# Kernel tuning notes

Measured on AMD Instinct MI355X. Metric: run time of the kernel, lower is better.

The kernel has to match this reference:

```python
import jax, jax.numpy as jnp
import numpy as np

HIDDEN = 2048
NUM_HEADS = 16
HEAD_DIM = HIDDEN // NUM_HEADS  # 128
SCALE = HEAD_DIM ** -0.5


def setup_inputs() -> dict:
    key = jax.random.key(0)
    ks = jax.random.split(key, 5)
    B, S = 2, 2048
    init = HIDDEN ** -0.5  # roughly kaiming-uniform scale for Linear weights
    return {
        "hidden_states": jax.random.normal(ks[0], (B, S, HIDDEN), dtype=jnp.float32),
        "Wq": jax.random.normal(ks[1], (HIDDEN, HIDDEN), dtype=jnp.float32) * init,
        "Wk": jax.random.normal(ks[2], (HIDDEN, HIDDEN), dtype=jnp.float32) * init,
        "Wv": jax.random.normal(ks[3], (HIDDEN, HIDDEN), dtype=jnp.float32) * init,
        "Wo": jax.random.normal(ks[4], (HIDDEN, HIDDEN), dtype=jnp.float32) * init,
    }


def reference(hidden_states, Wq, Wk, Wv, Wo):
    B, S, _ = hidden_states.shape
    # Projections (nn.Linear: x @ W.T; weights stored as [out, in])
    q = (hidden_states @ Wq.T).reshape(B, S, NUM_HEADS, HEAD_DIM).transpose(0, 2, 1, 3)
    k = (hidden_states @ Wk.T).reshape(B, S, NUM_HEADS, HEAD_DIM).transpose(0, 2, 1, 3)
    v = (hidden_states @ Wv.T).reshape(B, S, NUM_HEADS, HEAD_DIM).transpose(0, 2, 1, 3)
    # Full quadratic attention (faithful to the source's explicit materialization)
    scores = jnp.einsum("bhqd,bhkd->bhqk", q, k) * SCALE  # [B,H,S,S]
    probs = jax.nn.softmax(scores, axis=-1)
    attn = jnp.einsum("bhqk,bhkd->bhqd", probs, v)  # [B,H,S,Dh]
    attn = attn.transpose(0, 2, 1, 3).reshape(B, S, HIDDEN)
    return attn @ Wo.T
```

## Files before the change

### kernel.cpp

```cpp
#include <hip/hip_runtime.h>
#include <cstdint>

#define HIDDEN 2048
#define NHEADS 16
#define DH 128
#define BATCH 2
#define SEQ 2048
#define MTOT 4096
#define BH (BATCH * NHEADS)

typedef __attribute__((ext_vector_type(8))) short bf16x8;
typedef __attribute__((ext_vector_type(4))) float f32x4;

static constexpr float QSCALE = (float)(0.08838834764831845 * 1.4426950408889634);

__device__ __forceinline__ unsigned short f2bf(float f) {
  union { float f; uint32_t u; } v; v.f = f;
  uint32_t r = v.u + 0x7FFFu + ((v.u >> 16) & 1u);
  return (unsigned short)(r >> 16);
}
__device__ __forceinline__ uint32_t cvtpk(float lo, float hi) {
  uint32_t r;
  asm("v_cvt_pk_bf16_f32 %0, %1, %2" : "=v"(r) : "v"(lo), "v"(hi));
  return r;
}
__device__ __forceinline__ f32x4 mfma16(bf16x8 a, bf16x8 b, f32x4 c) {
  return __builtin_amdgcn_mfma_f32_16x16x32_bf16(a, b, c, 0, 0, 0);
}

typedef const __attribute__((address_space(1))) unsigned char* gas1_t;
typedef __attribute__((address_space(3))) unsigned char* las3_t;
__device__ __forceinline__ void gll16(const void* g, void* l) {
  __builtin_amdgcn_global_load_lds((gas1_t)g, (las3_t)l, 16, 0, 0);
}

template <int N>
__device__ __forceinline__ void waitvm() {
  if constexpr (N == 6) asm volatile("s_waitcnt vmcnt(6)" ::: "memory");
  else if constexpr (N == 3) asm volatile("s_waitcnt vmcnt(3)" ::: "memory");
  else asm volatile("s_waitcnt vmcnt(0)" ::: "memory");
}

__global__ __launch_bounds__(256) void cast_bf16_kernel(const float* __restrict__ in,
                                                        unsigned short* __restrict__ out,
                                                        int n) {
  int i = (blockIdx.x * 256 + threadIdx.x) * 4;
  if (i < n) {
    float4 f = *(const float4*)&in[i];
    ushort4 o;
    o.x = f2bf(f.x); o.y = f2bf(f.y); o.z = f2bf(f.z); o.w = f2bf(f.w);
    *(ushort4*)&out[i] = o;
  }
}

template <int VM>
__device__ __forceinline__ void gemm_body(int kt, char* SM,
                                          const unsigned short* pA,
                                          const unsigned short* pB0,
                                          const unsigned short* pB1,
                                          int wv, int wr, int wc, int g, int lr,
                                          f32x4 (&acc)[4][4]) {
  waitvm<VM>();
  __builtin_amdgcn_s_barrier();
  if (kt + 3 < 64) {
    char* slot = SM + ((kt + 3) & 3) * 24576;
    const size_t ko = (size_t)(kt + 3) * 32;
    gll16(pA + ko, slot + wv * 1024);
    gll16(pB0 + ko, slot + 8192 + wv * 1024);
    gll16(pB1 + ko, slot + 16384 + wv * 1024);
  }
  const char* Ac = SM + (kt & 3) * 24576;
  const char* Bc = Ac + 8192;
  const int fx = (lr >> 1) & 3;
  bf16x8 af[4], bfr[4];
#pragma unroll
  for (int mi = 0; mi < 4; ++mi)
    af[mi] = *(const bf16x8*)(Ac + (wr * 64 + mi * 16 + lr) * 64 + ((g ^ fx) * 16));
#pragma unroll
  for (int ni = 0; ni < 4; ++ni)
    bfr[ni] = *(const bf16x8*)(Bc + (wc * 64 + ni * 16 + lr) * 64 + ((g ^ fx) * 16));
  __builtin_amdgcn_s_setprio(1);
#pragma unroll
  for (int mi = 0; mi < 4; ++mi)
#pragma unroll
    for (int ni = 0; ni < 4; ++ni)
      acc[mi][ni] = mfma16(af[mi], bfr[ni], acc[mi][ni]);
  __builtin_amdgcn_s_setprio(0);
}

__global__ __launch_bounds__(512) void gemm_qkv_pipe(const unsigned short* __restrict__ A,
                                                     const unsigned short* __restrict__ Wq,
                                                     const unsigned short* __restrict__ Wk,
                                                     const unsigned short* __restrict__ Wv,
                                                     unsigned short* __restrict__ Qb,
                                                     unsigned short* __restrict__ Kb,
                                                     unsigned short* __restrict__ Vb) {
  __shared__ __align__(16) char SM[98304];
  const int tid = threadIdx.x;
  const int lane = tid & 63, wv = tid >> 6;
  const int wr = wv >> 2, wc = wv & 3;
  const int g = lane >> 4, lr = lane & 15;
  const int which = blockIdx.x >> 3;
  const int m0 = blockIdx.y * 128, n0 = (blockIdx.x & 7) * 256;
  const unsigned short* W = (which == 0) ? Wq : (which == 1) ? Wk : Wv;

  const int rA = tid >> 2, cA = (tid & 3) ^ ((rA >> 1) & 3);
  const unsigned short* pA = A + (size_t)(m0 + rA) * HIDDEN + cA * 8;
  const unsigned short* pB0 = W + (size_t)(n0 + rA) * HIDDEN + cA * 8;
  const unsigned short* pB1 = W + (size_t)(n0 + 128 + rA) * HIDDEN + cA * 8;

  f32x4 acc[4][4];
#pragma unroll
  for (int i = 0; i < 4; ++i)
#pragma unroll
    for (int j = 0; j < 4; ++j) acc[i][j] = (f32x4){0.f, 0.f, 0.f, 0.f};

#pragma unroll
  for (int t = 0; t < 3; ++t) {
    char* slot = SM + t * 24576;
    gll16(pA + t * 32, slot + wv * 1024);
    gll16(pB0 + t * 32, slot + 8192 + wv * 1024);
    gll16(pB1 + t * 32, slot + 16384 + wv * 1024);
  }

  for (int kt = 0; kt < 62; ++kt)
    gemm_body<6>(kt, SM, pA, pB0, pB1, wv, wr, wc, g, lr, acc);
  gemm_body<3>(62, SM, pA, pB0, pB1, wv, wr, wc, g, lr, acc);
  gemm_body<0>(63, SM, pA, pB0, pB1, wv, wr, wc, g, lr, acc);

  const float alpha = (which == 0) ? QSCALE : 1.0f;
  unsigned short* C = (which == 0) ? Qb : (which == 1) ? Kb : Vb;
#pragma unroll
  for (int mi = 0; mi < 4; ++mi)
#pragma unroll
    for (int ni = 0; ni < 4; ++ni)
#pragma unroll
      for (int r = 0; r < 4; ++r) {
        const int row = m0 + wr * 64 + mi * 16 + g * 4 + r;
        const int col = n0 + wc * 64 + ni * 16 + lr;
        const unsigned short v = f2bf(acc[mi][ni][r] * alpha);
        const int b = row >> 11, s = row & (SEQ - 1);
        const int h = col >> 7, d = col & (DH - 1);
        const size_t base = (size_t)(b * NHEADS + h) * SEQ * DH;
        if (which == 0)
          C[base + (size_t)s * DH + d] = v;
        else if (which == 1)
          C[base + (size_t)(s >> 5) * 4096 + (d >> 3) * 256 + (s & 31) * 8 + (d & 7)] = v;
        else
          C[base + (size_t)(s >> 3) * 1024 + d * 8 + (s & 7)] = v;
      }
}

__global__ __launch_bounds__(512) void gemm_out_pipe(const unsigned short* __restrict__ A,
                                                     const unsigned short* __restrict__ W,
                                                     float* __restrict__ C) {
  __shared__ __align__(16) char SM[98304];
  const int tid = threadIdx.x;
  const int lane = tid & 63, wv = tid >> 6;
  const int wr = wv >> 2, wc = wv & 3;
  const int g = lane >> 4, lr = lane & 15;
  const int m0 = blockIdx.y * 128, n0 = blockIdx.x * 256;

  const int rA = tid >> 2, cA = (tid & 3) ^ ((rA >> 1) & 3);
  const unsigned short* pA = A + (size_t)(m0 + rA) * HIDDEN + cA * 8;
  const unsigned short* pB0 = W + (size_t)(n0 + rA) * HIDDEN + cA * 8;
  const unsigned short* pB1 = W + (size_t)(n0 + 128 + rA) * HIDDEN + cA * 8;

  f32x4 acc[4][4];
#pragma unroll
  for (int i = 0; i < 4; ++i)
#pragma unroll
    for (int j = 0; j < 4; ++j) acc[i][j] = (f32x4){0.f, 0.f, 0.f, 0.f};

#pragma unroll
  for (int t = 0; t < 3; ++t) {
    char* slot = SM + t * 24576;
    gll16(pA + t * 32, slot + wv * 1024);
    gll16(pB0 + t * 32, slot + 8192 + wv * 1024);
    gll16(pB1 + t * 32, slot + 16384 + wv * 1024);
  }

  for (int kt = 0; kt < 62; ++kt)
    gemm_body<6>(kt, SM, pA, pB0, pB1, wv, wr, wc, g, lr, acc);
  gemm_body<3>(62, SM, pA, pB0, pB1, wv, wr, wc, g, lr, acc);
  gemm_body<0>(63, SM, pA, pB0, pB1, wv, wr, wc, g, lr, acc);

#pragma unroll
  for (int mi = 0; mi < 4; ++mi)
#pragma unroll
    for (int ni = 0; ni < 4; ++ni)
#pragma unroll
      for (int r = 0; r < 4; ++r) {
        const int row = m0 + wr * 64 + mi * 16 + g * 4 + r;
        const int col = n0 + wc * 64 + ni * 16 + lr;
        C[(size_t)row * HIDDEN + col] = acc[mi][ni][r];
      }
}

__global__ __launch_bounds__(256, 3) void attn_mfma(const unsigned short* __restrict__ Q,
                                                    const unsigned short* __restrict__ K,
                                                    const unsigned short* __restrict__ V,
                                                    unsigned short* __restrict__ Ab) {
  const int bid = blockIdx.x;
  const int bh = bid & 31;
  const int q0 = (bid >> 5) * 128;
  const int tid = threadIdx.x;
  const int wv = tid >> 6, lane = tid & 63;
  const int g = lane >> 4, lr = lane & 15;
  const unsigned short* Qh = Q + (size_t)bh * SEQ * DH;
  const unsigned short* Kh = K + (size_t)bh * SEQ * DH;
  const unsigned short* Vh = V + (size_t)bh * SEQ * DH;

  __shared__ __align__(16) unsigned short Kls[3][4096];
  __shared__ __align__(16) unsigned short Vls[3][4096];
  __shared__ __align__(16) unsigned short Pw[4][16][40];

  bf16x8 qf[2][4];
#pragma unroll
  for (int m = 0; m < 2; ++m)
#pragma unroll
    for (int kb = 0; kb < 4; ++kb)
      qf[m][kb] = *(const bf16x8*)&Qh[(size_t)(q0 + wv * 32 + m * 16 + lr) * DH +
                                      kb * 32 + g * 8];

  f32x4 acc[2][8];
#pragma unroll
  for (int m = 0; m < 2; ++m)
#pragma unroll
    for (int dn = 0; dn < 8; ++dn) acc[m][dn] = (f32x4){0.f, 0.f, 0.f, 0.f};
  float mrun[2] = {-1e30f, -1e30f};
  float lrun[2] = {0.f, 0.f};

#pragma unroll
  for (int tt = 0; tt < 2; ++tt)
#pragma unroll
    for (int j = 0; j < 2; ++j) {
      const int c = j * 256 + tid;
      gll16(Kh + (size_t)tt * 4096 + c * 8, (char*)&Kls[tt][0] + j * 4096 + wv * 1024);
      gll16(Vh + (size_t)tt * 4096 + c * 8, (char*)&Vls[tt][0] + j * 4096 + wv * 1024);
    }

  for (int t = 0; t < 64; ++t) {
    const int cur = t % 3;
    asm volatile("s_waitcnt vmcnt(4)" ::: "memory");
    __builtin_amdgcn_s_barrier();
    if (t + 2 < 64) {
      const int nx = (t + 2) % 3;
      const unsigned short* Kn = Kh + (size_t)(t + 2) * 4096;
      const unsigned short* Vn = Vh + (size_t)(t + 2) * 4096;
      char* kd = (char*)&Kls[nx][0];
      char* vd = (char*)&Vls[nx][0];
#pragma unroll
      for (int j = 0; j < 2; ++j) {
        const int c = j * 256 + tid;
        gll16(Kn + (size_t)c * 8, kd + j * 4096 + wv * 1024);
        gll16(Vn + (size_t)c * 8, vd + j * 4096 + wv * 1024);
      }
    }

    const char* Kc = (const char*)&Kls[cur][0];
    const char* Vc = (const char*)&Vls[cur][0];
    bf16x8 ap[2];
#pragma unroll
    for (int m = 0; m < 2; ++m) {
      f32x4 st0 = (f32x4){0.f, 0.f, 0.f, 0.f};
      f32x4 st1 = (f32x4){0.f, 0.f, 0.f, 0.f};
      __builtin_amdgcn_s_setprio(1);
#pragma unroll
      for (int kb = 0; kb < 4; ++kb) {
        const int cb = (kb * 4 + g) * 32;
        bf16x8 kf0 = *(const bf16x8*)(Kc + (cb + lr) * 16);
        bf16x8 kf1 = *(const bf16x8*)(Kc + (cb + 16 + lr) * 16);
        st0 = mfma16(kf0, qf[m][kb], st0);
        st1 = mfma16(kf1, qf[m][kb], st1);
      }
      __builtin_amdgcn_s_setprio(0);
      float mt = fmaxf(fmaxf(fmaxf(st0[0], st0[1]), fmaxf(st0[2], st0[3])),
                       fmaxf(fmaxf(st1[0], st1[1]), fmaxf(st1[2], st1[3])));
      mt = fmaxf(mt, __shfl_xor(mt, 16));
      mt = fmaxf(mt, __shfl_xor(mt, 32));
      if (!__all(mt <= mrun[m] + 8.0f)) {
        const float mnew = fmaxf(mrun[m], mt);
        const float corr = __builtin_amdgcn_exp2f(mrun[m] - mnew);
        lrun[m] *= corr;
        mrun[m] = mnew;
        const f32x4 cv = (f32x4){__shfl(corr, g * 4 + 0), __shfl(corr, g * 4 + 1),
                                 __shfl(corr, g * 4 + 2), __shfl(corr, g * 4 + 3)};
#pragma unroll
        for (int dn = 0; dn < 8; ++dn) acc[m][dn] *= cv;
      }
      float p[8], ls = 0.f;
#pragma unroll
      for (int r = 0; r < 4; ++r) {
        p[r] = __builtin_amdgcn_exp2f(st0[r] - mrun[m]);
        p[4 + r] = __builtin_amdgcn_exp2f(st1[r] - mrun[m]);
        ls += p[r] + p[4 + r];
      }
      lrun[m] += ls;
      uint2 pk0, pk1;
      pk0.x = cvtpk(p[0], p[1]); pk0.y = cvtpk(p[2], p[3]);
      pk1.x = cvtpk(p[4], p[5]); pk1.y = cvtpk(p[6], p[7]);
      *(uint2*)&Pw[wv][lr][4 * g] = pk0;
      *(uint2*)&Pw[wv][lr][16 + 4 * g] = pk1;
      ap[m] = *(const bf16x8*)&Pw[wv][lr][8 * g];
    }
    __builtin_amdgcn_s_setprio(1);
#pragma unroll
    for (int dn = 0; dn < 8; ++dn) {
      bf16x8 vf = *(const bf16x8*)(Vc + (g * 128 + dn * 16 + lr) * 16);
      acc[0][dn] = mfma16(ap[0], vf, acc[0][dn]);
      acc[1][dn] = mfma16(ap[1], vf, acc[1][dn]);
    }
    __builtin_amdgcn_s_setprio(0);
  }

  const int b = bh >> 4, h = bh & 15;
#pragma unroll
  for (int m = 0; m < 2; ++m) {
    lrun[m] += __shfl_xor(lrun[m], 16);
    lrun[m] += __shfl_xor(lrun[m], 32);
    const float inv = 1.f / lrun[m];
    float ir[4];
#pragma unroll
    for (int r = 0; r < 4; ++r) ir[r] = __shfl(inv, g * 4 + r);
#pragma unroll
    for (int dn = 0; dn < 8; ++dn)
#pragma unroll
      for (int r = 0; r < 4; ++r) {
        const int srow = q0 + wv * 32 + m * 16 + g * 4 + r;
        Ab[((size_t)(b * SEQ + srow) * NHEADS + h) * DH + dn * 16 + lr] =
            f2bf(acc[m][dn][r] * ir[r]);
      }
  }
}

extern "C" void kernel_launch(void* const* d_in, const int* in_sizes, int n_in,
                              void* d_out, int out_size, void* d_ws,
                              size_t ws_size, hipStream_t stream) {
  const float* X  = (const float*)d_in[0];
  const float* Wq = (const float*)d_in[1];
  const float* Wk = (const float*)d_in[2];
  const float* Wv = (const float*)d_in[3];
  const float* Wo = (const float*)d_in[4];
  float* out = (float*)d_out;

  const int n1 = MTOT * HIDDEN;
  const int n2 = HIDDEN * HIDDEN;

  char* p = (char*)d_ws;
  unsigned short* Xb  = (unsigned short*)(p + 0);
  unsigned short* Qb  = (unsigned short*)(p + 16777216);
  unsigned short* Kb  = (unsigned short*)(p + 33554432);
  unsigned short* Vb  = (unsigned short*)(p + 50331648);
  unsigned short* Wqb = (unsigned short*)(p + 67108864);
  unsigned short* Wkb = (unsigned short*)(p + 75497472);
  unsigned short* Wvb = (unsigned short*)(p + 83886080);
  unsigned short* Wob = (unsigned short*)(p + 92274688);
  unsigned short* Ab  = (unsigned short*)(p + 100663296);

  cast_bf16_kernel<<<n1 / 1024, 256, 0, stream>>>(X, Xb, n1);
  cast_bf16_kernel<<<n2 / 1024, 256, 0, stream>>>(Wq, Wqb, n2);
  cast_bf16_kernel<<<n2 / 1024, 256, 0, stream>>>(Wk, Wkb, n2);
  cast_bf16_kernel<<<n2 / 1024, 256, 0, stream>>>(Wv, Wvb, n2);
  cast_bf16_kernel<<<n2 / 1024, 256, 0, stream>>>(Wo, Wob, n2);

  gemm_qkv_pipe<<<dim3(24, MTOT / 128), 512, 0, stream>>>(Xb, Wqb, Wkb, Wvb,
                                                          Qb, Kb, Vb);

  attn_mfma<<<dim3(512), 256, 0, stream>>>(Qb, Kb, Vb, Ab);

  gemm_out_pipe<<<dim3(HIDDEN / 256, MTOT / 128), 512, 0, stream>>>(Ab, Wob, out);
}
```

Baseline: 287.6 us.

## Deepen GEMM K-tile to 64 with split-phase prefetch and merge cast kernels

The two projection GEMMs move from 32-wide K tiles with a 4-slot ring to 64-wide K tiles with a 3-slot ring. Each tile is processed in two half-K phases, and the global-to-LDS prefetch is interleaved between the phases, with a new XOR swizzle for 128-byte rows. The five fp32-to-bf16 cast launches are merged into one kernel. The aim is fewer barriers per K element and less launch overhead, at the cost of 144KB of LDS per block and more barriers inside each step.

```diff
diff --git a/kernel.cpp b/kernel.cpp
--- a/kernel.cpp
+++ b/kernel.cpp
@@ -37,48 +37,59 @@
 template <int N>
 __device__ __forceinline__ void waitvm() {
   if constexpr (N == 6) asm volatile("s_waitcnt vmcnt(6)" ::: "memory");
-  else if constexpr (N == 3) asm volatile("s_waitcnt vmcnt(3)" ::: "memory");
-  else asm volatile("s_waitcnt vmcnt(0)" ::: "memory");
-}
-
-__global__ __launch_bounds__(256) void cast_bf16_kernel(const float* __restrict__ in,
-                                                        unsigned short* __restrict__ out,
-                                                        int n) {
-  int i = (blockIdx.x * 256 + threadIdx.x) * 4;
-  if (i < n) {
-    float4 f = *(const float4*)&in[i];
-    ushort4 o;
-    o.x = f2bf(f.x); o.y = f2bf(f.y); o.z = f2bf(f.z); o.w = f2bf(f.w);
-    *(ushort4*)&out[i] = o;
+  else if constexpr (N == 0) asm volatile("s_waitcnt vmcnt(0)" ::: "memory");
+}
+
+__global__ __launch_bounds__(256) void cast_all(
+    const float* __restrict__ X, const float* __restrict__ Wq,
+    const float* __restrict__ Wk, const float* __restrict__ Wv,
+    const float* __restrict__ Wo, unsigned short* __restrict__ Xb,
+    unsigned short* __restrict__ Wqb, unsigned short* __restrict__ Wkb,
+    unsigned short* __restrict__ Wvb, unsigned short* __restrict__ Wob) {
+  const int n1 = MTOT * HIDDEN;
+  const int i = (blockIdx.x * 256 + threadIdx.x) * 4;
+  const float* s;
+  unsigned short* d;
+  int o;
+  if (i < n1) {
+    s = X; d = Xb; o = i;
+  } else {
+    const int j = i - n1;
+    const int w = j >> 22;
+    o = j & ((1 << 22) - 1);
+    s = (w == 0) ? Wq : (w == 1) ? Wk : (w == 2) ? Wv : Wo;
+    d = (w == 0) ? Wqb : (w == 1) ? Wkb : (w == 2) ? Wvb : Wob;
   }
-}
-
-template <int VM>
-__device__ __forceinline__ void gemm_body(int kt, char* SM,
-                                          const unsigned short* pA,
-                                          const unsigned short* pB0,
-                                          const unsigned short* pB1,
-                                          int wv, int wr, int wc, int g, int lr,
-                                          f32x4 (&acc)[4][4]) {
-  waitvm<VM>();
+  float4 f = *(const float4*)&s[o];
+  ushort4 u;
+  u.x = f2bf(f.x); u.y = f2bf(f.y); u.z = f2bf(f.z); u.w = f2bf(f.w);
+  *(ushort4*)&d[o] = u;
+}
+
+template <int VM, bool PF>
+__device__ __forceinline__ void pipe_body(
+    int kt, char* SM, const unsigned short* aS0, const unsigned short* aS1,
+    const unsigned short* bS0, const unsigned short* bS1,
+    const unsigned short* bS2, const unsigned short* bS3, int wv, int wr,
+    int wc, int g, int lr, f32x4 (&acc)[4][4]) {
+  const char* Ac = SM + (kt % 3) * 49152;
+  const char* Bc = Ac + 16384;
+  char* slot2 = SM + ((kt + 2) % 3) * 49152;
+  const size_t ko = (size_t)(kt + 2) * 64;
+  const int rx = lr & 7;
+  bf16x8 af[4], bfr[4];
+#pragma unroll
+  for (int mi = 0; mi < 4; ++mi)
+    af[mi] = *(const bf16x8*)(Ac + (wr * 64 + mi * 16 + lr) * 128 + ((g ^ rx) * 16));
+#pragma unroll
+  for (int ni = 0; ni < 4; ++ni)
+    bfr[ni] = *(const bf16x8*)(Bc + (wc * 64 + ni * 16 + lr) * 128 + ((g ^ rx) * 16));
+  if (PF) {
+    gll16(aS0 + ko, slot2 + wv * 2048);
+    gll16(aS1 + ko, slot2 + wv * 2048 + 1024);
+    gll16(bS0 + ko, slot2 + 16384 + wv * 4096);
+  }
   __builtin_amdgcn_s_barrier();
-  if (kt + 3 < 64) {
-    char* slot = SM + ((kt + 3) & 3) * 24576;
-    const size_t ko = (size_t)(kt + 3) * 32;
-    gll16(pA + ko, slot + wv * 1024);
-    gll16(pB0 + ko, slot + 8192 + wv * 1024);
-    gll16(pB1 + ko, slot + 16384 + wv * 1024);
-  }
-  const char* Ac = SM + (kt & 3) * 24576;
-  const char* Bc = Ac + 8192;
-  const int fx = (lr >> 1) & 3;
-  bf16x8 af[4], bfr[4];
-#pragma unroll
-  for (int mi = 0; mi < 4; ++mi)
-    af[mi] = *(const bf16x8*)(Ac + (wr * 64 + mi * 16 + lr) * 64 + ((g ^ fx) * 16));
-#pragma unroll
-  for (int ni = 0; ni < 4; ++ni)
-    bfr[ni] = *(const bf16x8*)(Bc + (wc * 64 + ni * 16 + lr) * 64 + ((g ^ fx) * 16));
   __builtin_amdgcn_s_setprio(1);
 #pragma unroll
   for (int mi = 0; mi < 4; ++mi)
@@ -86,16 +97,76 @@
     for (int ni = 0; ni < 4; ++ni)
       acc[mi][ni] = mfma16(af[mi], bfr[ni], acc[mi][ni]);
   __builtin_amdgcn_s_setprio(0);
-}
-
-__global__ __launch_bounds__(512) void gemm_qkv_pipe(const unsigned short* __restrict__ A,
-                                                     const unsigned short* __restrict__ Wq,
-                                                     const unsigned short* __restrict__ Wk,
-                                                     const unsigned short* __restrict__ Wv,
-                                                     unsigned short* __restrict__ Qb,
-                                                     unsigned short* __restrict__ Kb,
-                                                     unsigned short* __restrict__ Vb) {
-  __shared__ __align__(16) char SM[98304];
+  __builtin_amdgcn_s_barrier();
+#pragma unroll
+  for (int mi = 0; mi < 4; ++mi)
+    af[mi] = *(const bf16x8*)(Ac + (wr * 64 + mi * 16 + lr) * 128 + (((4 + g) ^ rx) * 16));
+#pragma unroll
+  for (int ni = 0; ni < 4; ++ni)
+    bfr[ni] = *(const bf16x8*)(Bc + (wc * 64 + ni * 16 + lr) * 128 + (((4 + g) ^ rx) * 16));
+  if (PF) {
+    gll16(bS1 + ko, slot2 + 16384 + wv * 4096 + 1024);
+    gll16(bS2 + ko, slot2 + 16384 + wv * 4096 + 2048);
+    gll16(bS3 + ko, slot2 + 16384 + wv * 4096 + 3072);
+  }
+  __builtin_amdgcn_s_barrier();
+  __builtin_amdgcn_s_setprio(1);
+#pragma unroll
+  for (int mi = 0; mi < 4; ++mi)
+#pragma unroll
+    for (int ni = 0; ni < 4; ++ni)
+      acc[mi][ni] = mfma16(af[mi], bfr[ni], acc[mi][ni]);
+  __builtin_amdgcn_s_setprio(0);
+  if (VM >= 0) waitvm<VM>();
+  __builtin_amdgcn_s_barrier();
+}
+
+#define PIPE_SETUP(Abase, Bbase)                                              \
+  const int idxA0 = wv * 128 + lane, idxA1 = idxA0 + 64;                      \
+  const int rA0 = idxA0 >> 3, cA0 = (idxA0 & 7) ^ (rA0 & 7);                  \
+  const int rA1 = idxA1 >> 3, cA1 = (idxA1 & 7) ^ (rA1 & 7);                  \
+  const unsigned short* aS0 = (Abase) + (size_t)(m0 + rA0) * HIDDEN + cA0 * 8;\
+  const unsigned short* aS1 = (Abase) + (size_t)(m0 + rA1) * HIDDEN + cA1 * 8;\
+  const int idxB0 = wv * 256 + lane, idxB1 = idxB0 + 64,                      \
+            idxB2 = idxB0 + 128, idxB3 = idxB0 + 192;                         \
+  const int rB0 = idxB0 >> 3, cB0 = (idxB0 & 7) ^ (rB0 & 7);                  \
+  const int rB1 = idxB1 >> 3, cB1 = (idxB1 & 7) ^ (rB1 & 7);                  \
+  const int rB2 = idxB2 >> 3, cB2 = (idxB2 & 7) ^ (rB2 & 7);                  \
+  const int rB3 = idxB3 >> 3, cB3 = (idxB3 & 7) ^ (rB3 & 7);                  \
+  const unsigned short* bS0 = (Bbase) + (size_t)(n0 + rB0) * HIDDEN + cB0 * 8;\
+  const unsigned short* bS1 = (Bbase) + (size_t)(n0 + rB1) * HIDDEN + cB1 * 8;\
+  const unsigned short* bS2 = (Bbase) + (size_t)(n0 + rB2) * HIDDEN + cB2 * 8;\
+  const unsigned short* bS3 = (Bbase) + (size_t)(n0 + rB3) * HIDDEN + cB3 * 8;
+
+#define PIPE_PROLOGUE()                                                       \
+  _Pragma("unroll") for (int tt = 0; tt < 2; ++tt) {                          \
+    char* slot = SM + tt * 49152;                                             \
+    const size_t ko = (size_t)tt * 64;                                        \
+    gll16(aS0 + ko, slot + wv * 2048);                                        \
+    gll16(aS1 + ko, slot + wv * 2048 + 1024);                                 \
+    gll16(bS0 + ko, slot + 16384 + wv * 4096);                                \
+    gll16(bS1 + ko, slot + 16384 + wv * 4096 + 1024);                         \
+    gll16(bS2 + ko, slot + 16384 + wv * 4096 + 2048);                         \
+    gll16(bS3 + ko, slot + 16384 + wv * 4096 + 3072);                         \
+  }                                                                           \
+  waitvm<6>();                                                                \
+  __builtin_amdgcn_s_barrier();
+
+#define PIPE_LOOP()                                                           \
+  for (int kt = 0; kt < 30; ++kt)                                             \
+    pipe_body<6, true>(kt, SM, aS0, aS1, bS0, bS1, bS2, bS3, wv, wr, wc, g,   \
+                       lr, acc);                                              \
+  pipe_body<0, false>(30, SM, aS0, aS1, bS0, bS1, bS2, bS3, wv, wr, wc, g,    \
+                      lr, acc);                                               \
+  pipe_body<-1, false>(31, SM, aS0, aS1, bS0, bS1, bS2, bS3, wv, wr, wc, g,   \
+                       lr, acc);
+
+__global__ __launch_bounds__(512) void gemm_qkv_pipe(
+    const unsigned short* __restrict__ A, const unsigned short* __restrict__ Wq,
+    const unsigned short* __restrict__ Wk, const unsigned short* __restrict__ Wv,
+    unsigned short* __restrict__ Qb, unsigned short* __restrict__ Kb,
+    unsigned short* __restrict__ Vb) {
+  __shared__ __align__(16) char SM[147456];
   const int tid = threadIdx.x;
   const int lane = tid & 63, wv = tid >> 6;
   const int wr = wv >> 2, wc = wv & 3;
@@ -104,10 +175,7 @@
   const int m0 = blockIdx.y * 128, n0 = (blockIdx.x & 7) * 256;
   const unsigned short* W = (which == 0) ? Wq : (which == 1) ? Wk : Wv;
 
-  const int rA = tid >> 2, cA = (tid & 3) ^ ((rA >> 1) & 3);
-  const unsigned short* pA = A + (size_t)(m0 + rA) * HIDDEN + cA * 8;
-  const unsigned short* pB0 = W + (size_t)(n0 + rA) * HIDDEN + cA * 8;
-  const unsigned short* pB1 = W + (size_t)(n0 + 128 + rA) * HIDDEN + cA * 8;
+  PIPE_SETUP(A, W)
 
   f32x4 acc[4][4];
 #pragma unroll
@@ -115,18 +183,8 @@
 #pragma unroll
     for (int j = 0; j < 4; ++j) acc[i][j] = (f32x4){0.f, 0.f, 0.f, 0.f};
 
-#pragma unroll
-  for (int t = 0; t < 3; ++t) {
-    char* slot = SM + t * 24576;
-    gll16(pA + t * 32, slot + wv * 1024);
-    gll16(pB0 + t * 32, slot + 8192 + wv * 1024);
-    gll16(pB1 + t * 32, slot + 16384 + wv * 1024);
-  }
-
-  for (int kt = 0; kt < 62; ++kt)
-    gemm_body<6>(kt, SM, pA, pB0, pB1, wv, wr, wc, g, lr, acc);
-  gemm_body<3>(62, SM, pA, pB0, pB1, wv, wr, wc, g, lr, acc);
-  gemm_body<0>(63, SM, pA, pB0, pB1, wv, wr, wc, g, lr, acc);
+  PIPE_PROLOGUE()
+  PIPE_LOOP()
 
   const float alpha = (which == 0) ? QSCALE : 1.0f;
   unsigned short* C = (which == 0) ? Qb : (which == 1) ? Kb : Vb;
@@ -151,20 +209,17 @@
       }
 }
 
-__global__ __launch_bounds__(512) void gemm_out_pipe(const unsigned short* __restrict__ A,
-                                                     const unsigned short* __restrict__ W,
-                                                     float* __restrict__ C) {
-  __shared__ __align__(16) char SM[98304];
+__global__ __launch_bounds__(512) void gemm_out_pipe(
+    const unsigned short* __restrict__ A, const unsigned short* __restrict__ W,
+    float* __restrict__ C) {
+  __shared__ __align__(16) char SM[147456];
   const int tid = threadIdx.x;
   const int lane = tid & 63, wv = tid >> 6;
   const int wr = wv >> 2, wc = wv & 3;
   const int g = lane >> 4, lr = lane & 15;
   const int m0 = blockIdx.y * 128, n0 = blockIdx.x * 256;
 
-  const int rA = tid >> 2, cA = (tid & 3) ^ ((rA >> 1) & 3);
-  const unsigned short* pA = A + (size_t)(m0 + rA) * HIDDEN + cA * 8;
-  const unsigned short* pB0 = W + (size_t)(n0 + rA) * HIDDEN + cA * 8;
-  const unsigned short* pB1 = W + (size_t)(n0 + 128 + rA) * HIDDEN + cA * 8;
+  PIPE_SETUP(A, W)
 
   f32x4 acc[4][4];
 #pragma unroll
@@ -172,18 +227,8 @@
 #pragma unroll
     for (int j = 0; j < 4; ++j) acc[i][j] = (f32x4){0.f, 0.f, 0.f, 0.f};
 
-#pragma unroll
-  for (int t = 0; t < 3; ++t) {
-    char* slot = SM + t * 24576;
-    gll16(pA + t * 32, slot + wv * 1024);
-    gll16(pB0 + t * 32, slot + 8192 + wv * 1024);
-    gll16(pB1 + t * 32, slot + 16384 + wv * 1024);
-  }
-
-  for (int kt = 0; kt < 62; ++kt)
-    gemm_body<6>(kt, SM, pA, pB0, pB1, wv, wr, wc, g, lr, acc);
-  gemm_body<3>(62, SM, pA, pB0, pB1, wv, wr, wc, g, lr, acc);
-  gemm_body<0>(63, SM, pA, pB0, pB1, wv, wr, wc, g, lr, acc);
+  PIPE_PROLOGUE()
+  PIPE_LOOP()
 
 #pragma unroll
   for (int mi = 0; mi < 4; ++mi)
@@ -358,11 +403,8 @@
   unsigned short* Wob = (unsigned short*)(p + 92274688);
   unsigned short* Ab  = (unsigned short*)(p + 100663296);
 
-  cast_bf16_kernel<<<n1 / 1024, 256, 0, stream>>>(X, Xb, n1);
-  cast_bf16_kernel<<<n2 / 1024, 256, 0, stream>>>(Wq, Wqb, n2);
-  cast_bf16_kernel<<<n2 / 1024, 256, 0, stream>>>(Wk, Wkb, n2);
-  cast_bf16_kernel<<<n2 / 1024, 256, 0, stream>>>(Wv, Wvb, n2);
-  cast_bf16_kernel<<<n2 / 1024, 256, 0, stream>>>(Wo, Wob, n2);
+  cast_all<<<(n1 + 4 * n2) / 1024, 256, 0, stream>>>(X, Wq, Wk, Wv, Wo, Xb, Wqb,
+                                                     Wkb, Wvb, Wob);
 
   gemm_qkv_pipe<<<dim3(24, MTOT / 128), 512, 0, stream>>>(Xb, Wqb, Wkb, Wvb,
                                                           Qb, Kb, Vb);
```

Result: faster. 272.7 us (-5.2%).
